# Kernel optimization log

Hardware: AMD Instinct MI355X
Metric: run time of the kernel (lower is better)

Reference implementation:

```python
import jax, jax.numpy as jnp
import numpy as np

# static config (mirrors init_kwargs)
FS = 512          # frame_seqlen
NFPB = 2          # num_frame_per_block
NIB = 3           # num image/action/state blocks
NAPB = 32         # num_action_per_block
NSPB = 1          # num_state_per_block
LOCAL = 4         # local_attn_size (frames)
FIRST = FS
IMGB = NIB * NFPB * FS
ALEN = NIB * NAPB
SLEN = NIB * NSPB
TOTAL = FIRST + IMGB + ALEN + SLEN   # 3683
DIM = 1536
NH = 12
HD = DIM // NH    # 128
EPS = 1e-6


def _build_mask():
    # faithful port of _visualize_attention_mask (the block-sparse pattern)
    m = np.zeros((TOTAL, TOTAL), dtype=bool)
    fi0, fi1 = 0, FIRST
    ib0, ib1 = fi1, fi1 + IMGB
    a0, a1 = ib1, ib1 + ALEN
    s0 = a1
    m[fi0:fi1, fi0:fi1] = True  # first image: self only (sink)
    for b in range(NIB):
        bs = ib0 + b * NFPB * FS
        be = ib0 + (b + 1) * NFPB * FS
        m[bs:be, fi0:fi1] = True                      # sink
        kv = max(ib0, be - LOCAL * FS)                # local window
        m[bs:be, kv:be] = True
        m[bs:be, a0 + b * NAPB:a0 + (b + 1) * NAPB] = True
        m[bs:be, s0 + b * NSPB:s0 + (b + 1) * NSPB] = True
    for b in range(NIB):
        ab0 = a0 + b * NAPB
        ab1 = a0 + (b + 1) * NAPB
        m[ab0:ab1, fi0:fi1] = True
        ibe = ib0 + (b + 1) * NFPB * FS
        kv = max(ib0, ibe - LOCAL * FS)
        m[ab0:ab1, kv:ibe] = True
        m[ab0:ab1, ab0:ab1] = True
        m[ab0:ab1, s0 + b * NSPB:s0 + (b + 1) * NSPB] = True
    for b in range(NIB):
        ss = s0 + b * NSPB
        se = s0 + (b + 1) * NSPB
        m[ss:se, ss:se] = True
    return m

_MASK = jnp.asarray(_build_mask())


def _rms_norm(x, g):
    # WanRMSNorm over full dim, fp32 accumulation
    v = jnp.mean(jnp.square(x.astype(jnp.float32)), axis=-1, keepdims=True)
    return (x.astype(jnp.float32) * jax.lax.rsqrt(v + EPS)).astype(x.dtype) * g


def _rope(x, cos, sin):
    # x: [B,L,n,hd]; pairs are consecutive (..., hd//2, 2)
    B, L, n, d = x.shape
    xp = x.reshape(B, L, n, d // 2, 2)
    xr, xi = xp[..., 0], xp[..., 1]
    c = cos[None, :, None, :]
    s = sin[None, :, None, :]
    yr = xr * c - xi * s
    yi = xr * s + xi * c
    return jnp.stack([yr, yi], axis=-1).reshape(B, L, n, d)


def setup_inputs() -> dict:
    key = jax.random.key(0)
    ks = jax.random.split(key, 16)
    x = jax.random.normal(ks[0], (1, TOTAL, DIM), jnp.float32)

    def mkfreq(k, L):
        ang = jax.random.uniform(k, (L, HD // 2), jnp.float32, 0.0, 2.0 * np.pi)
        return jnp.stack([jnp.cos(ang), jnp.sin(ang)], axis=-1).reshape(L, HD)

    freqs = mkfreq(ks[1], FIRST + IMGB)
    freqs_action = mkfreq(ks[2], ALEN)
    freqs_state = mkfreq(ks[3], SLEN)
    sc = 1.0 / np.sqrt(DIM)
    Wq = jax.random.normal(ks[4], (DIM, DIM), jnp.float32) * sc
    Wk = jax.random.normal(ks[5], (DIM, DIM), jnp.float32) * sc
    Wv = jax.random.normal(ks[6], (DIM, DIM), jnp.float32) * sc
    Wo = jax.random.normal(ks[7], (DIM, DIM), jnp.float32) * sc
    bq = jax.random.normal(ks[8], (DIM,), jnp.float32) * 0.01
    bk = jax.random.normal(ks[9], (DIM,), jnp.float32) * 0.01
    bv = jax.random.normal(ks[10], (DIM,), jnp.float32) * 0.01
    bo = jax.random.normal(ks[11], (DIM,), jnp.float32) * 0.01
    gq = jnp.ones((DIM,), jnp.float32)
    gk = jnp.ones((DIM,), jnp.float32)
    return {"x": x, "freqs": freqs, "freqs_action": freqs_action,
            "freqs_state": freqs_state, "Wq": Wq, "bq": bq, "Wk": Wk, "bk": bk,
            "Wv": Wv, "bv": bv, "Wo": Wo, "bo": bo, "gq": gq, "gk": gk}


def reference(x, freqs, freqs_action, freqs_state, Wq, bq, Wk, bk, Wv, bv, Wo, bo, gq, gk):
    B, L, _ = x.shape
    q = _rms_norm(x @ Wq + bq, gq).reshape(B, L, NH, HD)
    k = _rms_norm(x @ Wk + bk, gk).reshape(B, L, NH, HD)
    v = (x @ Wv + bv).reshape(B, L, NH, HD)
    # full-sequence rope: image freqs then action freqs then state freqs
    f = jnp.concatenate([freqs, freqs_action, freqs_state], axis=0).reshape(L, HD // 2, 2)
    cos, sin = f[..., 0], f[..., 1]
    q = _rope(q, cos, sin)
    k = _rope(k, cos, sin)
    scores = jnp.einsum('bqnd,bknd->bnqk', q, k) / np.sqrt(HD)
    scores = jnp.where(_MASK[None, None], scores, jnp.finfo(scores.dtype).min)
    p = jax.nn.softmax(scores, axis=-1)
    o = jnp.einsum('bnqk,bknd->bqnd', p, v).reshape(B, L, DIM)
    return o @ Wo + bo
```

## Files before the change

kernel.cpp:

```cpp
#include <hip/hip_runtime.h>

#define LSEQ 3683
#define LPAD 3840
#define DIMSZ 1536
#define NHEAD 12
#define HEADD 128
#define SM_SCALE 0.088388347648318447f

typedef unsigned short u16;
typedef unsigned int u32;
typedef __bf16 bf16x8 __attribute__((ext_vector_type(8)));
typedef float f32x4 __attribute__((ext_vector_type(4)));

__device__ __forceinline__ u16 f2b(float f) {
  u32 u = __float_as_uint(f);
  u += 0x7FFFu + ((u >> 16) & 1u);
  return (u16)(u >> 16);
}
__device__ __forceinline__ float b2f(u16 s) {
  return __uint_as_float(((u32)s) << 16);
}
__device__ __forceinline__ int imax(int a, int b) { return a > b ? a : b; }

__device__ __forceinline__ void gl_lds16(const u16* g, u16* l) {
  __builtin_amdgcn_global_load_lds((const __attribute__((address_space(1))) u32*)g,
                                   (__attribute__((address_space(3))) u32*)l,
                                   16, 0, 0);
}

__device__ __forceinline__ int xcd_swz(int orig, int nwg) {
  int q = nwg >> 3, r = nwg & 7;
  int x = orig & 7, l = orig >> 3;
  return (x < r ? x * (q + 1) : r * (q + 1) + (x - r) * q) + l;
}

#define CONV_BLOCKS 5760
__global__ void prep_kernel(const float* __restrict__ x, u16* __restrict__ xb,
                            const float* __restrict__ W0, const float* __restrict__ W1,
                            const float* __restrict__ W2, const float* __restrict__ W3,
                            u16* __restrict__ Wt) {
  __shared__ float tile[32][33];
  int bx = blockIdx.x;
  if (bx < CONV_BLOCKS) {
    long idx = (long)bx * blockDim.x + threadIdx.x;
    long base = idx * 4;
    if (base >= (long)LPAD * DIMSZ) return;
    float4 v;
    if (base < (long)LSEQ * DIMSZ) v = *(const float4*)(x + base);
    else v = make_float4(0.f, 0.f, 0.f, 0.f);
    ushort4 o;
    o.x = f2b(v.x); o.y = f2b(v.y); o.z = f2b(v.z); o.w = f2b(v.w);
    *(ushort4*)(xb + base) = o;
  } else {
    int i = bx - CONV_BLOCKS;
    int z = i / 2304;
    int r = i % 2304;
    int bxx = r % 48, byy = r / 48;
    const float* W = (z == 0) ? W0 : (z == 1) ? W1 : (z == 2) ? W2 : W3;
    u16* dst = Wt + (size_t)z * DIMSZ * DIMSZ;
    int k0 = bxx * 32, n0 = byy * 32;
    int tx = threadIdx.x & 31, ty = threadIdx.x >> 5;
    #pragma unroll
    for (int q = 0; q < 4; q++) {
      int k = k0 + ty + q * 8;
      tile[ty + q * 8][tx] = W[(size_t)k * DIMSZ + n0 + tx];
    }
    __syncthreads();
    #pragma unroll
    for (int q = 0; q < 4; q++) {
      int n = n0 + ty + q * 8;
      dst[(size_t)n * DIMSZ + k0 + tx] = f2b(tile[tx][ty + q * 8]);
    }
  }
}

#define BAR() __builtin_amdgcn_s_barrier()
#define LGK0() asm volatile("s_waitcnt lgkmcnt(0)" ::: "memory")
#define LGK8() asm volatile("s_waitcnt lgkmcnt(8)" ::: "memory")
#define VMC9() asm volatile("s_waitcnt vmcnt(9)" ::: "memory")
#define VMC6() asm volatile("s_waitcnt vmcnt(6)" ::: "memory")
#define VMC0() asm volatile("s_waitcnt vmcnt(0)" ::: "memory")
#define PRIO1() __builtin_amdgcn_s_setprio(1)
#define PRIO0() __builtin_amdgcn_s_setprio(0)

#define STG_A(buf, q, kt) \
  gl_lds16(gA + (size_t)((q) * 64) * DIMSZ + (kt), &Asg[buf][((q) * 64 + w * 8) * 64]);
#define STG_B(buf, q, kt) \
  gl_lds16(gB + (size_t)((q) * 64) * DIMSZ + (kt), &Bsg[buf][((q) * 64 + w * 8) * 64]);

#define LDA3(buf, mh) { \
  _Pragma("unroll") for (int mf = 0; mf < 3; mf++) { \
    int rb = (wm * 96 + (mh) * 48 + mf * 16) * 64; \
    Ar[mf * 2 + 0] = *(const bf16x8*)&Asg[buf][rb + off0]; \
    Ar[mf * 2 + 1] = *(const bf16x8*)&Asg[buf][rb + off1]; } }
#define LDB3(buf, nh) { \
  _Pragma("unroll") for (int nf = 0; nf < 3; nf++) { \
    int rb = (wn * 96 + (nh) * 48 + nf * 16) * 64; \
    Br[nh][nf * 2 + 0] = *(const bf16x8*)&Bsg[buf][rb + off0]; \
    Br[nh][nf * 2 + 1] = *(const bf16x8*)&Bsg[buf][rb + off1]; } }

#define MFMAQ3(mh, nh) { \
  _Pragma("unroll") for (int mf = 0; mf < 3; mf++) \
    _Pragma("unroll") for (int nf = 0; nf < 3; nf++) { \
      acc[(mh)*3+mf][(nh)*3+nf] = __builtin_amdgcn_mfma_f32_16x16x32_bf16(Ar[mf*2+0], Br[nh][nf*2+0], acc[(mh)*3+mf][(nh)*3+nf], 0, 0, 0); \
      acc[(mh)*3+mf][(nh)*3+nf] = __builtin_amdgcn_mfma_f32_16x16x32_bf16(Ar[mf*2+1], Br[nh][nf*2+1], acc[(mh)*3+mf][(nh)*3+nf], 0, 0, 0); } }

#define GEMM384_BODY() \
  STG_B(0, 0, 0) STG_B(0, 1, 0) STG_B(0, 2, 0) \
  STG_A(0, 0, 0) STG_A(0, 1, 0) STG_A(0, 2, 0) \
  STG_A(0, 3, 0) STG_A(0, 4, 0) STG_A(0, 5, 0) \
  STG_B(1, 0, 64) STG_B(1, 1, 64) STG_B(1, 2, 64) \
  STG_A(1, 0, 64) STG_A(1, 1, 64) STG_A(1, 2, 64) \
  STG_A(1, 3, 64) STG_A(1, 4, 64) STG_A(1, 5, 64) \
  VMC9(); \
  BAR(); \
  for (int i = 0; i < DIMSZ / 64 / 2 - 1; ++i) { \
    int kt2 = (2 * i + 2) * 64; \
    int kt3 = (2 * i + 3) * 64; \
    LDA3(0, 0) LDB3(0, 0) \
    LGK8(); BAR(); LGK0(); \
    PRIO1(); MFMAQ3(0, 0) PRIO0(); \
    BAR(); \
    LDB3(0, 1) \
    BAR(); LGK0(); \
    PRIO1(); MFMAQ3(0, 1) PRIO0(); \
    BAR(); \
    LDA3(0, 1) \
    STG_B(0, 0, kt2) STG_B(0, 1, kt2) STG_B(0, 2, kt2) \
    BAR(); LGK0(); \
    PRIO1(); MFMAQ3(1, 1) PRIO0(); \
    BAR(); \
    STG_A(0, 0, kt2) STG_A(0, 1, kt2) STG_A(0, 2, kt2) \
    VMC6(); BAR(); \
    PRIO1(); MFMAQ3(1, 0) PRIO0(); \
    BAR(); \
    LDA3(1, 0) LDB3(1, 0) \
    STG_A(0, 3, kt2) STG_A(0, 4, kt2) STG_A(0, 5, kt2) \
    LGK8(); BAR(); LGK0(); \
    PRIO1(); MFMAQ3(0, 0) PRIO0(); \
    BAR(); \
    LDB3(1, 1) \
    BAR(); LGK0(); \
    PRIO1(); MFMAQ3(0, 1) PRIO0(); \
    BAR(); \
    LDA3(1, 1) \
    STG_B(1, 0, kt3) STG_B(1, 1, kt3) STG_B(1, 2, kt3) \
    BAR(); LGK0(); \
    PRIO1(); MFMAQ3(1, 1) PRIO0(); \
    BAR(); \
    STG_A(1, 0, kt3) STG_A(1, 1, kt3) STG_A(1, 2, kt3) \
    STG_A(1, 3, kt3) STG_A(1, 4, kt3) STG_A(1, 5, kt3) \
    VMC9(); BAR(); \
    PRIO1(); MFMAQ3(1, 0) PRIO0(); \
    BAR(); \
  } \
  { \
    LDA3(0, 0) LDB3(0, 0) \
    LGK8(); BAR(); LGK0(); \
    PRIO1(); MFMAQ3(0, 0) PRIO0(); \
    BAR(); \
    LDB3(0, 1) \
    BAR(); LGK0(); \
    PRIO1(); MFMAQ3(0, 1) PRIO0(); \
    BAR(); \
    LDA3(0, 1) \
    BAR(); LGK0(); \
    PRIO1(); MFMAQ3(1, 1) PRIO0(); \
    BAR(); \
    VMC0(); BAR(); \
    PRIO1(); MFMAQ3(1, 0) PRIO0(); \
    BAR(); \
    LDA3(1, 0) LDB3(1, 0) \
    LGK8(); BAR(); LGK0(); \
    PRIO1(); MFMAQ3(0, 0) PRIO0(); \
    BAR(); \
    LDB3(1, 1) \
    BAR(); LGK0(); \
    PRIO1(); MFMAQ3(0, 1) PRIO0(); \
    BAR(); \
    LDA3(1, 1) \
    BAR(); LGK0(); \
    PRIO1(); MFMAQ3(1, 1) PRIO0(); \
    MFMAQ3(1, 0) \
  }

__launch_bounds__(512, 2)
__global__ void gemm_qkv384_kernel(const u16* __restrict__ A, const u16* __restrict__ Wt,
                                   const float* __restrict__ bq, const float* __restrict__ bk,
                                   const float* __restrict__ bv,
                                   u16* __restrict__ Qb, u16* __restrict__ Kb,
                                   u16* __restrict__ Vt) {
  __shared__ __align__(16) u16 Asg[2][384 * 64];
  __shared__ __align__(16) u16 Bsg[2][192 * 64];

  int wg = xcd_swz(blockIdx.x, 10 * 24);
  int nt = wg % 24;
  int m0 = (wg / 24) * 384;
  int which = nt >> 3;
  const float* bias = (which == 0) ? bq : (which == 1) ? bk : bv;

  int t = threadIdx.x;
  int lane = t & 63, w = t >> 6;
  int c = lane & 15, g = lane >> 4;
  int wm = w >> 1, wn = w & 1;

  int srow = t >> 3;
  int schunk = ((t & 7) ^ (srow & 7)) * 8;
  const u16* gA = A + (size_t)(m0 + srow) * DIMSZ + schunk;
  const u16* gB = Wt + (size_t)(nt * 192 + srow) * DIMSZ + schunk;

  int off0 = c * 64 + ((g) ^ (c & 7)) * 8;
  int off1 = c * 64 + ((g + 4) ^ (c & 7)) * 8;

  f32x4 acc[6][6];
  f32x4 zero = {0.f, 0.f, 0.f, 0.f};
  #pragma unroll
  for (int am = 0; am < 6; am++)
    #pragma unroll
    for (int an = 0; an < 6; an++) acc[am][an] = zero;
  bf16x8 Ar[6];
  bf16x8 Br[2][6];

  GEMM384_BODY()

  #pragma unroll
  for (int an = 0; an < 6; an++) {
    int ncol = (nt & 7) * 192 + wn * 96 + (an / 3) * 48 + (an % 3) * 16 + c;
    float bvv = bias[ncol];
    #pragma unroll
    for (int am = 0; am < 6; am++) {
      int rowb = m0 + wm * 96 + (am / 3) * 48 + (am % 3) * 16 + 4 * g;
      if (which == 2) {
        ushort4 pv;
        pv.x = f2b(acc[am][an][0] + bvv);
        pv.y = f2b(acc[am][an][1] + bvv);
        pv.z = f2b(acc[am][an][2] + bvv);
        pv.w = f2b(acc[am][an][3] + bvv);
        *(ushort4*)&Vt[(size_t)ncol * LPAD + rowb] = pv;
      } else {
        u16* P = (which == 1) ? Kb : Qb;
        #pragma unroll
        for (int r = 0; r < 4; r++)
          P[(size_t)(rowb + r) * DIMSZ + ncol] = f2b(acc[am][an][r] + bvv);
      }
    }
  }
}

__launch_bounds__(512, 2)
__global__ void gemm_out384_kernel(const u16* __restrict__ A, const u16* __restrict__ Bt,
                                   const float* __restrict__ bias, float* __restrict__ outF) {
  __shared__ __align__(16) u16 Asg[2][384 * 64];
  __shared__ __align__(16) u16 Bsg[2][192 * 64];

  int wg = xcd_swz(blockIdx.x, 10 * 8);
  int nt = wg % 8;
  int m0 = (wg / 8) * 384;

  int t = threadIdx.x;
  int lane = t & 63, w = t >> 6;
  int c = lane & 15, g = lane >> 4;
  int wm = w >> 1, wn = w & 1;

  int srow = t >> 3;
  int schunk = ((t & 7) ^ (srow & 7)) * 8;
  const u16* gA = A + (size_t)(m0 + srow) * DIMSZ + schunk;
  const u16* gB = Bt + (size_t)(nt * 192 + srow) * DIMSZ + schunk;

  int off0 = c * 64 + ((g) ^ (c & 7)) * 8;
  int off1 = c * 64 + ((g + 4) ^ (c & 7)) * 8;

  f32x4 acc[6][6];
  f32x4 zero = {0.f, 0.f, 0.f, 0.f};
  #pragma unroll
  for (int am = 0; am < 6; am++)
    #pragma unroll
    for (int an = 0; an < 6; an++) acc[am][an] = zero;
  bf16x8 Ar[6];
  bf16x8 Br[2][6];

  GEMM384_BODY()

  #pragma unroll
  for (int an = 0; an < 6; an++) {
    int ncol = nt * 192 + wn * 96 + (an / 3) * 48 + (an % 3) * 16 + c;
    float bvv = bias[ncol];
    #pragma unroll
    for (int am = 0; am < 6; am++) {
      int rowb = m0 + wm * 96 + (am / 3) * 48 + (am % 3) * 16 + 4 * g;
      #pragma unroll
      for (int r = 0; r < 4; r++) {
        int row = rowb + r;
        if (row < LSEQ) outF[(size_t)row * DIMSZ + ncol] = acc[am][an][r] + bvv;
      }
    }
  }
}

__launch_bounds__(256)
__global__ void normrope_kernel(u16* __restrict__ Qb, u16* __restrict__ Kb,
                                const float* __restrict__ gq, const float* __restrict__ gk,
                                const float* __restrict__ freqs, const float* __restrict__ freqs_a,
                                const float* __restrict__ freqs_s) {
  int l = blockIdx.x;
  int sel = blockIdx.y;
  u16* P = sel ? Kb : Qb;
  const float* gvec = sel ? gk : gq;
  int t = threadIdx.x;
  u16* row = P + (size_t)l * DIMSZ;
  float xv[6];
  #pragma unroll
  for (int i = 0; i < 3; i++) {
    int p = i * 256 + t;
    ushort2 u = *(const ushort2*)(row + 2 * p);
    xv[2 * i] = b2f(u.x);
    xv[2 * i + 1] = b2f(u.y);
  }
  float ss = 0.f;
  #pragma unroll
  for (int i = 0; i < 6; i++) ss += xv[i] * xv[i];
  #pragma unroll
  for (int d = 32; d; d >>= 1) ss += __shfl_down(ss, d);
  __shared__ float red[4];
  __shared__ float rshare;
  if ((t & 63) == 0) red[t >> 6] = ss;
  __syncthreads();
  if (t == 0) rshare = rsqrtf((red[0] + red[1] + red[2] + red[3]) * (1.0f / DIMSZ) + 1e-6f);
  __syncthreads();
  float rms = rshare;

  const float* f = (l < 3584) ? (freqs + (size_t)l * HEADD)
                : (l < 3680) ? (freqs_a + (size_t)(l - 3584) * HEADD)
                             : (freqs_s + (size_t)(l - 3680) * HEADD);
  #pragma unroll
  for (int i = 0; i < 3; i++) {
    int p = i * 256 + t;
    int j = p & 63;
    float2 csn = *(const float2*)(f + 2 * j);
    float2 gv = *(const float2*)(gvec + 2 * p);
    float xr = xv[2 * i] * rms * gv.x;
    float xi = xv[2 * i + 1] * rms * gv.y;
    ushort2 o;
    o.x = f2b(xr * csn.x - xi * csn.y);
    o.y = f2b(xr * csn.y + xi * csn.x);
    *(ushort2*)(row + 2 * p) = o;
  }
}

#define PSLOT_U16 16640
#define NTAIL 84
__launch_bounds__(256, 2)
__global__ void attn_fused_kernel(const u16* __restrict__ Q, const u16* __restrict__ K,
                                  const u16* __restrict__ Vt, u16* __restrict__ O,
                                  u16* __restrict__ DP, float* __restrict__ Part) {
  __shared__ __align__(16) u16 Ks[2][32 * 136];
  __shared__ __align__(16) u16 Vs[2][128 * 40];
  __shared__ __align__(16) u16 Pl[4][32 * 40];

  int t = threadIdx.x, lane = t & 63, w = t >> 6, g = lane >> 4, c = lane & 15;
  const float c1 = SM_SCALE * 1.44269504088896340f;
  const float c2 = 12.0f * 1.44269504088896340f;

  f32x4 zero = {0.f, 0.f, 0.f, 0.f};
  bf16x8 onesv;
  {
    u16 ob = 0x3F80;
    #pragma unroll
    for (int i = 0; i < 8; i++) onesv[i] = ((const __bf16*)&ob)[0];
  }

  if (blockIdx.x < NTAIL) {
    char* smem = (char*)&Ks[0][0];
    float* Lsum = (float*)(smem + 20608);

    int j = blockIdx.x;
    int bxx = j % 7;
    int h = j / 7;
    int qt, part;
    if (bxx < 3) { qt = 112 + bxx; part = 0; }
    else if (bxx < 6) { qt = 112 + (bxx - 3); part = 1; }
    else { qt = 115; part = 0; }
    int qbase = qt * 32;
    bool heavy = (qt <= 114);

    int S0, E0, S1, E1, S2, E2, S3, E3, niv;
    if (qbase < 3680) {
      int b = (qbase - 3584) >> 5;
      int ibe = 512 + (b + 1) * 1024;
      int kv = imax(512, ibe - 2048);
      S0 = 0; E0 = 512; S1 = kv; E1 = ibe;
      S2 = 3584 + 32 * b; E2 = S2 + 32; S3 = 3680 + b; E3 = S3 + 1; niv = 4;
    } else {
      S0 = 3680; E0 = 3683; S1 = S2 = S3 = 0; E1 = E2 = E3 = 0; niv = 1;
    }
    bool diag = (qbase >= 3680);

    int B0 = S0 & ~31, B1 = S1 & ~31, B2 = S2 & ~31, B3 = S3 & ~31;
    int T1 = (E0 - B0 + 31) >> 5;
    int T2 = T1 + ((niv > 1) ? ((E1 - B1 + 31) >> 5) : 0);
    int T3 = T2 + ((niv > 2) ? ((E2 - B2 + 31) >> 5) : 0);
    int T4 = T3 + ((niv > 3) ? ((E3 - B3 + 31) >> 5) : 0);
    int ntile = T4;

    int rlo = 0, rhi = ntile;
    if (heavy) { int half = (ntile + 1) >> 1; if (part == 0) rhi = half; else rlo = half; }

    auto tile_of = [&](int f, int& k0, int& lo, int& hi) {
      k0 = B0 + (f << 5); lo = S0; hi = E0;
      if (niv > 1 && f >= T1) { k0 = B1 + ((f - T1) << 5); lo = S1; hi = E1; }
      if (niv > 2 && f >= T2) { k0 = B2 + ((f - T2) << 5); lo = S2; hi = E2; }
      if (niv > 3 && f >= T3) { k0 = B3 + ((f - T3) << 5); lo = S3; hi = E3; }
    };

    bf16x8 qf[2][4];
    #pragma unroll
    for (int a = 0; a < 2; a++) {
      const u16* qp = Q + (size_t)(qbase + a * 16 + c) * DIMSZ + h * HEADD + 8 * g;
      #pragma unroll
      for (int s = 0; s < 4; s++) qf[a][s] = *(const bf16x8*)(qp + 32 * s);
    }

    f32x4 acc[2][8];
    f32x4 lacc[2];
    #pragma unroll
    for (int a = 0; a < 2; a++) {
      lacc[a] = zero;
      #pragma unroll
      for (int cc = 0; cc < 8; cc++) acc[a][cc] = zero;
    }

    u16* PwA = (u16*)smem + w * 2560;
    u16* PwB = PwA + 1280;

    bf16x8 kc[2][4], vbuf[8], pa0, pa1;

    auto loadK = [&](int k0) {
      #pragma unroll
      for (int k2 = 0; k2 < 2; k2++) {
        const u16* kp = K + (size_t)(k0 + 16 * k2 + c) * DIMSZ + h * HEADD + 8 * g;
        #pragma unroll
        for (int s = 0; s < 4; s++) kc[k2][s] = *(const bf16x8*)(kp + 32 * s);
      }
    };
    auto loadV = [&](int k0) {
      #pragma unroll
      for (int cc = 0; cc < 8; cc++)
        vbuf[cc] = *(const bf16x8*)(Vt + (size_t)(h * HEADD + cc * 16 + c) * LPAD + k0 + 8 * g);
    };
    auto QKf = [&](f32x4 (&sc)[2][2]) {
      sc[0][0] = zero; sc[0][1] = zero; sc[1][0] = zero; sc[1][1] = zero;
      #pragma unroll
      for (int k2 = 0; k2 < 2; k2++)
        #pragma unroll
        for (int s = 0; s < 4; s++) {
          sc[0][k2] = __builtin_amdgcn_mfma_f32_16x16x32_bf16(qf[0][s], kc[k2][s], sc[0][k2], 0, 0, 0);
          sc[1][k2] = __builtin_amdgcn_mfma_f32_16x16x32_bf16(qf[1][s], kc[k2][s], sc[1][k2], 0, 0, 0);
        }
    };
    auto smstore = [&](f32x4 (&sc)[2][2], int k0, int lo, int hi, u16* Pw) {
      #pragma unroll
      for (int a = 0; a < 2; a++)
        #pragma unroll
        for (int k2 = 0; k2 < 2; k2++) {
          int k = k0 + k2 * 16 + c;
          bool valid = (k >= lo) && (k < hi);
          #pragma unroll
          for (int r = 0; r < 4; r++) {
            float p = __builtin_amdgcn_exp2f(sc[a][k2][r] * c1 - c2);
            bool v = valid;
            if (diag) { int qr = qbase + a * 16 + 4 * g + r; v = v && (k == qr); }
            Pw[(a * 16 + 4 * g + r) * 40 + k2 * 16 + c] = v ? f2b(p) : (u16)0;
          }
        }
    };
    auto readP = [&](u16* Pw) {
      pa0 = *(const bf16x8*)&Pw[c * 40 + 8 * g];
      pa1 = *(const bf16x8*)&Pw[(16 + c) * 40 + 8 * g];
    };
    auto PV = [&]() {
      #pragma unroll
      for (int cc = 0; cc < 8; cc++) {
        acc[0][cc] = __builtin_amdgcn_mfma_f32_16x16x32_bf16(pa0, vbuf[cc], acc[0][cc], 0, 0, 0);
        acc[1][cc] = __builtin_amdgcn_mfma_f32_16x16x32_bf16(pa1, vbuf[cc], acc[1][cc], 0, 0, 0);
      }
      lacc[0] = __builtin_amdgcn_mfma_f32_16x16x32_bf16(pa0, onesv, lacc[0], 0, 0, 0);
      lacc[1] = __builtin_amdgcn_mfma_f32_16x16x32_bf16(pa1, onesv, lacc[1], 0, 0, 0);
    };

    int i = rlo + w;
    if (i < rhi) {
      int ik0, ilo, ihi; tile_of(i, ik0, ilo, ihi);
      loadK(ik0);
      loadV(ik0);
      {
        f32x4 sc[2][2]; QKf(sc);
        smstore(sc, ik0, ilo, ihi, PwA);
      }
      asm volatile("s_waitcnt lgkmcnt(0)" ::: "memory");
      __builtin_amdgcn_sched_barrier(0);
      readP(PwA);
      int nx = i + 4;
      int nk0 = 0, nlo = 0, nhi = 0;
      bool useB = true;
      if (nx < rhi) { tile_of(nx, nk0, nlo, nhi); loadK(nk0); }
      while (nx < rhi) {
        int ck0 = nk0, clo = nlo, chi = nhi;
        f32x4 sc[2][2]; QKf(sc);
        int nn = nx + 4;
        if (nn < rhi) { tile_of(nn, nk0, nlo, nhi); loadK(nk0); }
        u16* Pw = useB ? PwB : PwA;
        smstore(sc, ck0, clo, chi, Pw);
        PV();
        loadV(ck0);
        asm volatile("s_waitcnt lgkmcnt(0)" ::: "memory");
        __builtin_amdgcn_sched_barrier(0);
        readP(Pw);
        useB = !useB;
        i = nx; nx = nn;
      }
      PV();
    }

    __syncthreads();
    float* Oacc = (float*)smem;
    if (w == 0) {
      #pragma unroll
      for (int a = 0; a < 2; a++) {
        #pragma unroll
        for (int cc = 0; cc < 8; cc++)
          #pragma unroll
          for (int r = 0; r < 4; r++)
            Oacc[(a * 16 + 4 * g + r) * 132 + cc * 16 + c] = acc[a][cc][r];
        if (c == 0)
          #pragma unroll
          for (int r = 0; r < 4; r++) Lsum[a * 16 + 4 * g + r] = lacc[a][r];
      }
    }
    __syncthreads();
    #pragma unroll
    for (int ww = 1; ww < 4; ww++) {
      if (w == ww) {
        #pragma unroll
        for (int a = 0; a < 2; a++) {
          #pragma unroll
          for (int cc = 0; cc < 8; cc++)
            #pragma unroll
            for (int r = 0; r < 4; r++)
              Oacc[(a * 16 + 4 * g + r) * 132 + cc * 16 + c] += acc[a][cc][r];
          if (c == 0)
            #pragma unroll
            for (int r = 0; r < 4; r++) Lsum[a * 16 + 4 * g + r] += lacc[a][r];
        }
      }
      __syncthreads();
    }

    int row = t >> 3, c0 = (t & 7) * 16;
    if (heavy) {
      size_t slot = ((size_t)((qt - 112) * 12 + h)) * 2 + part;
      float* P = Part + slot * 4160;
      #pragma unroll
      for (int jj = 0; jj < 16; jj += 4)
        *(float4*)&P[row * 128 + c0 + jj] = *(float4*)&Oacc[row * 132 + c0 + jj];
      if ((t & 7) == 0) P[4096 + row] = Lsum[row];
    } else {
      int orow = qbase + row;
      if (orow < LSEQ) {
        float lsv = Lsum[row];
        float inv = (lsv > 0.f) ? 1.0f / lsv : 0.f;
        u16 tmp[16];
        #pragma unroll
        for (int jj = 0; jj < 16; jj++) tmp[jj] = f2b(Oacc[row * 132 + c0 + jj] * inv);
        u16* op = O + (size_t)orow * DIMSZ + h * HEADD + c0;
        *(uint4*)(op) = *(uint4*)&tmp[0];
        *(uint4*)(op + 8) = *(uint4*)&tmp[8];
      }
    }
    return;
  }

  int bx = blockIdx.x - NTAIL;
  int qbase, h, part, nparts, fb;
  if (bx < 48) { qbase = (bx / 12) * 128; h = bx % 12; part = 0; nparts = 1; fb = -1; }
  else if (bx < 336) { int i = bx - 48; int qb = i / 36; h = (i / 3) % 12; part = i % 3; nparts = 3; fb = 0; qbase = 512 + qb * 128; }
  else if (bx < 720) { int i = bx - 336; int qb = i / 48; h = (i / 4) % 12; part = i % 4; nparts = 4; fb = 1; qbase = 1536 + qb * 128; }
  else { int i = bx - 720; int qb = i / 48; h = (i / 4) % 12; part = i % 4; nparts = 4; fb = 2; qbase = 2560 + qb * 128; }

  int S0, E0, S1, E1, S2, E2, S3, E3, niv;
  if (fb < 0) { S0 = 0; E0 = 512; S1 = E1 = S2 = E2 = S3 = E3 = 0; niv = 1; }
  else {
    int be = 512 + (fb + 1) * 1024;
    int kv = imax(512, be - 2048);
    S0 = 0; E0 = 512; S1 = kv; E1 = be;
    S2 = 3584 + 32 * fb; E2 = S2 + 32; S3 = 3680 + fb; E3 = S3 + 1; niv = 4;
  }
  int B0 = S0 & ~31, B1 = S1 & ~31, B2 = S2 & ~31, B3 = S3 & ~31;
  int T1 = (E0 - B0 + 31) >> 5;
  int T2 = T1 + ((niv > 1) ? ((E1 - B1 + 31) >> 5) : 0);
  int T3 = T2 + ((niv > 2) ? ((E2 - B2 + 31) >> 5) : 0);
  int T4 = T3 + ((niv > 3) ? ((E3 - B3 + 31) >> 5) : 0);
  int ntile = T4;
  int rlo = (ntile * part) / nparts, rhi = (ntile * (part + 1)) / nparts;

  auto tile_of = [&](int f, int& k0, int& lo, int& hi) {
    k0 = B0 + (f << 5); lo = S0; hi = E0;
    if (niv > 1 && f >= T1) { k0 = B1 + ((f - T1) << 5); lo = S1; hi = E1; }
    if (niv > 2 && f >= T2) { k0 = B2 + ((f - T2) << 5); lo = S2; hi = E2; }
    if (niv > 3 && f >= T3) { k0 = B3 + ((f - T3) << 5); lo = S3; hi = E3; }
  };

  const u16* kgp = K + (size_t)(t >> 3) * DIMSZ + h * HEADD + 8 * (t & 7);
  int kds = (t >> 3) * 136 + 8 * (t & 7);
  const u16* vgp = Vt + ((size_t)h * HEADD + (t >> 1)) * LPAD + 16 * (t & 1);
  int vds = (t >> 1) * 40 + 16 * (t & 1);

  uint4 sk0, sk1, sv0, sv1;
  auto stage_load = [&](int k0) {
    const u16* kp = kgp + (size_t)k0 * DIMSZ;
    sk0 = *(const uint4*)(kp);
    sk1 = *(const uint4*)(kp + 64);
    sv0 = *(const uint4*)(vgp + k0);
    sv1 = *(const uint4*)(vgp + k0 + 8);
  };
  auto stage_write = [&](int buf) {
    *(uint4*)&Ks[buf][kds] = sk0;
    *(uint4*)&Ks[buf][kds + 64] = sk1;
    *(uint4*)&Vs[buf][vds] = sv0;
    *(uint4*)&Vs[buf][vds + 8] = sv1;
  };

  int qrow0 = qbase + 32 * w;
  bf16x8 qf[2][4];
  #pragma unroll
  for (int a = 0; a < 2; a++) {
    const u16* qp = Q + (size_t)(qrow0 + a * 16 + c) * DIMSZ + h * HEADD + 8 * g;
    #pragma unroll
    for (int s = 0; s < 4; s++) qf[a][s] = *(const bf16x8*)(qp + 32 * s);
  }

  f32x4 acc[2][8];
  f32x4 lacc[2];
  #pragma unroll
  for (int a = 0; a < 2; a++) {
    lacc[a] = zero;
    #pragma unroll
    for (int cc = 0; cc < 8; cc++) acc[a][cc] = zero;
  }

  u16* Pw = &Pl[w][0];
  __bf16* Pwh = (__bf16*)Pw;

  {
    int k0, lo, hi; tile_of(rlo, k0, lo, hi);
    stage_load(k0);
    stage_write(0);
  }
  __syncthreads();
  int cur = 0;

  for (int tt = rlo; tt < rhi; ++tt) {
    int ck0, clo, chi; tile_of(tt, ck0, clo, chi);
    bool pre = (tt + 1 < rhi);
    if (pre) { int nk0, nl, nh; tile_of(tt + 1, nk0, nl, nh); stage_load(nk0); }

    f32x4 sc[2][2];
    sc[0][0] = zero; sc[0][1] = zero; sc[1][0] = zero; sc[1][1] = zero;
    #pragma unroll
    for (int k2 = 0; k2 < 2; k2++)
      #pragma unroll
      for (int s = 0; s < 4; s++) {
        bf16x8 kf = *(const bf16x8*)&Ks[cur][(16 * k2 + c) * 136 + 32 * s + 8 * g];
        sc[0][k2] = __builtin_amdgcn_mfma_f32_16x16x32_bf16(qf[0][s], kf, sc[0][k2], 0, 0, 0);
        sc[1][k2] = __builtin_amdgcn_mfma_f32_16x16x32_bf16(qf[1][s], kf, sc[1][k2], 0, 0, 0);
      }

    if (ck0 >= clo && ck0 + 32 <= chi) {
      #pragma unroll
      for (int a = 0; a < 2; a++)
        #pragma unroll
        for (int k2 = 0; k2 < 2; k2++)
          #pragma unroll
          for (int r = 0; r < 4; r++) {
            float p = __builtin_amdgcn_exp2f(sc[a][k2][r] * c1 - c2);
            Pwh[(a * 16 + 4 * g + r) * 40 + k2 * 16 + c] = (__bf16)p;
          }
    } else {
      #pragma unroll
      for (int a = 0; a < 2; a++)
        #pragma unroll
        for (int k2 = 0; k2 < 2; k2++) {
          int k = ck0 + k2 * 16 + c;
          bool valid = (k >= clo) && (k < chi);
          #pragma unroll
          for (int r = 0; r < 4; r++) {
            float p = __builtin_amdgcn_exp2f(sc[a][k2][r] * c1 - c2);
            Pwh[(a * 16 + 4 * g + r) * 40 + k2 * 16 + c] = valid ? (__bf16)p : (__bf16)0.0f;
          }
        }
    }
    asm volatile("s_waitcnt lgkmcnt(0)" ::: "memory");
    __builtin_amdgcn_sched_barrier(0);

    bf16x8 pa0 = *(const bf16x8*)&Pw[c * 40 + 8 * g];
    bf16x8 pa1 = *(const bf16x8*)&Pw[(16 + c) * 40 + 8 * g];

    #pragma unroll
    for (int cc = 0; cc < 8; cc++) {
      bf16x8 vf = *(const bf16x8*)&Vs[cur][(cc * 16 + c) * 40 + 8 * g];
      acc[0][cc] = __builtin_amdgcn_mfma_f32_16x16x32_bf16(pa0, vf, acc[0][cc], 0, 0, 0);
      acc[1][cc] = __builtin_amdgcn_mfma_f32_16x16x32_bf16(pa1, vf, acc[1][cc], 0, 0, 0);
    }
    lacc[0] = __builtin_amdgcn_mfma_f32_16x16x32_bf16(pa0, onesv, lacc[0], 0, 0, 0);
    lacc[1] = __builtin_amdgcn_mfma_f32_16x16x32_bf16(pa1, onesv, lacc[1], 0, 0, 0);

    if (pre) stage_write(cur ^ 1);
    __syncthreads();
    cur ^= 1;
  }

  if (nparts == 1) {
    float inv[2][4];
    #pragma unroll
    for (int a = 0; a < 2; a++)
      #pragma unroll
      for (int r = 0; r < 4; r++) inv[a][r] = (lacc[a][r] > 0.f) ? 1.0f / lacc[a][r] : 0.f;
    #pragma unroll
    for (int a = 0; a < 2; a++)
      #pragma unroll
      for (int cc = 0; cc < 8; cc++)
        #pragma unroll
        for (int r = 0; r < 4; r++) {
          int row = qrow0 + a * 16 + 4 * g + r;
          O[(size_t)row * DIMSZ + h * HEADD + cc * 16 + c] = f2b(acc[a][cc][r] * inv[a][r]);
        }
  } else {
    int qb = (qbase - 512 - fb * 1024) >> 7;
    int sbase = (fb == 0) ? 0 : (fb == 1 ? 288 : 672);
    int slot = sbase + (qb * 12 + h) * nparts + part;
    u16* DPs = DP + (size_t)slot * PSLOT_U16;
    float* lout = (float*)(DPs + 16384);
    #pragma unroll
    for (int a = 0; a < 2; a++) {
      #pragma unroll
      for (int cc = 0; cc < 8; cc++)
        #pragma unroll
        for (int r = 0; r < 4; r++)
          DPs[(32 * w + a * 16 + 4 * g + r) * 128 + cc * 16 + c] = f2b(acc[a][cc][r]);
      if (c == 0)
        #pragma unroll
        for (int r = 0; r < 4; r++) lout[32 * w + a * 16 + 4 * g + r] = lacc[a][r];
    }
  }
}

__launch_bounds__(256)
__global__ void attn_merge_kernel(const u16* __restrict__ DP, const float* __restrict__ Part,
                                  u16* __restrict__ O) {
  int bx = blockIdx.x, h = blockIdx.y;
  int T = threadIdx.x;
  if (bx < 24) {
    int qi = bx;
    int fb = qi >> 3, qb = qi & 7;
    int nparts = (fb == 0) ? 3 : 4;
    int sbase = (fb == 0) ? 0 : (fb == 1 ? 288 : 672);
    int slot0 = sbase + (qb * 12 + h) * nparts;
    int qbase = 512 + fb * 1024 + qb * 128;
    int row = T >> 1, c0 = 64 * (T & 1);

    float sum[64];
    #pragma unroll
    for (int j = 0; j < 64; j++) sum[j] = 0.f;
    float l = 0.f;
    for (int p = 0; p < nparts; p++) {
      const u16* S = DP + (size_t)(slot0 + p) * PSLOT_U16;
      l += ((const float*)(S + 16384))[row];
      #pragma unroll
      for (int j = 0; j < 64; j += 8) {
        uint4 v = *(const uint4*)&S[row * 128 + c0 + j];
        const u16* pv = (const u16*)&v;
        #pragma unroll
        for (int q = 0; q < 8; q++) sum[j + q] += b2f(pv[q]);
      }
    }
    float inv = (l > 0.f) ? 1.0f / l : 0.f;
    u16 tmp[64];
    #pragma unroll
    for (int j = 0; j < 64; j++) tmp[j] = f2b(sum[j] * inv);
    u16* op = O + (size_t)(qbase + row) * DIMSZ + h * HEADD + c0;
    #pragma unroll
    for (int j = 0; j < 64; j += 8) *(uint4*)(op + j) = *(uint4*)&tmp[j];
  } else {
    int b = bx - 24;
    const float* A = Part + ((size_t)(b * 12 + h)) * 2 * 4160;
    const float* B = A + 4160;
    int row = T >> 3, c0 = (T & 7) * 16;
    float l = A[4096 + row] + B[4096 + row];
    float inv = (l > 0.f) ? 1.0f / l : 0.f;
    int orow = 3584 + b * 32 + row;
    u16 tmp[16];
    #pragma unroll
    for (int jj = 0; jj < 16; jj += 4) {
      float4 va = *(const float4*)&A[row * 128 + c0 + jj];
      float4 vb = *(const float4*)&B[row * 128 + c0 + jj];
      tmp[jj + 0] = f2b((va.x + vb.x) * inv);
      tmp[jj + 1] = f2b((va.y + vb.y) * inv);
      tmp[jj + 2] = f2b((va.z + vb.z) * inv);
      tmp[jj + 3] = f2b((va.w + vb.w) * inv);
    }
    u16* op = O + (size_t)orow * DIMSZ + h * HEADD + c0;
    *(uint4*)(op) = *(uint4*)&tmp[0];
    *(uint4*)(op + 8) = *(uint4*)&tmp[8];
  }
}

extern "C" void kernel_launch(void* const* d_in, const int* in_sizes, int n_in,
                              void* d_out, int out_size, void* d_ws, size_t ws_size,
                              hipStream_t stream) {
  (void)in_sizes; (void)n_in; (void)out_size; (void)ws_size;
  const float* x       = (const float*)d_in[0];
  const float* freqs   = (const float*)d_in[1];
  const float* freqs_a = (const float*)d_in[2];
  const float* freqs_s = (const float*)d_in[3];
  const float* Wq = (const float*)d_in[4];
  const float* bq = (const float*)d_in[5];
  const float* Wk = (const float*)d_in[6];
  const float* bk = (const float*)d_in[7];
  const float* Wv = (const float*)d_in[8];
  const float* bv = (const float*)d_in[9];
  const float* Wo = (const float*)d_in[10];
  const float* bo = (const float*)d_in[11];
  const float* gq = (const float*)d_in[12];
  const float* gk = (const float*)d_in[13];
  float* out = (float*)d_out;

  char* ws = (char*)d_ws;
  size_t off = 0;
  auto alloc = [&](size_t bytes) -> void* {
    void* p = ws + off;
    off += (bytes + 255) & ~(size_t)255;
    return p;
  };
  u16* xb   = (u16*)alloc((size_t)LPAD * DIMSZ * 2);
  u16* Wt   = (u16*)alloc((size_t)4 * DIMSZ * DIMSZ * 2);
  u16* Qb   = (u16*)alloc((size_t)LPAD * DIMSZ * 2);
  u16* Kb   = (u16*)alloc((size_t)LPAD * DIMSZ * 2);
  u16* Vt   = (u16*)alloc((size_t)DIMSZ * LPAD * 2);
  u16* Ob   = (u16*)alloc((size_t)LPAD * DIMSZ * 2);
  u16* DP   = (u16*)alloc((size_t)1056 * PSLOT_U16 * 2);
  float* PartT = (float*)alloc((size_t)3 * 12 * 2 * 4160 * 4);

  prep_kernel<<<dim3(CONV_BLOCKS + 9216), 256, 0, stream>>>(x, xb, Wq, Wk, Wv, Wo, Wt);

  gemm_qkv384_kernel<<<dim3(240), 512, 0, stream>>>(xb, Wt, bq, bk, bv, Qb, Kb, Vt);

  normrope_kernel<<<dim3(LSEQ, 2), 256, 0, stream>>>(Qb, Kb, gq, gk, freqs, freqs_a, freqs_s);

  attn_fused_kernel<<<dim3(NTAIL + 1104), 256, 0, stream>>>(Qb, Kb, Vt, Ob, DP, PartT);
  attn_merge_kernel<<<dim3(27, 12), 256, 0, stream>>>(DP, PartT, Ob);

  gemm_out384_kernel<<<dim3(80), 512, 0, stream>>>(Ob, Wt + 3 * (size_t)DIMSZ * DIMSZ, bo, out);
}
```

Baseline: 238.7 us.

## Drop software pipelining in attention loop to raise occupancy to three blocks

Replaces the software-pipelined K/V prefetch loop, which used double-buffered P tiles and a full 8-register V buffer, with a simple per-tile loop. V is loaded and consumed in two halves, and the launch bound is raised from 2 to 3 blocks per SM. The intent is to cut register pressure so more waves are resident and can hide memory latency. In exchange, the explicit overlap of the next tile's K load with current compute is lost, so global loads are now exposed inside each iteration.

```diff
diff --git a/kernel.cpp b/kernel.cpp
--- a/kernel.cpp
+++ b/kernel.cpp
@@ -349,7 +349,7 @@
 
 #define PSLOT_U16 16640
 #define NTAIL 84
-__launch_bounds__(256, 2)
+__launch_bounds__(256, 3)
 __global__ void attn_fused_kernel(const u16* __restrict__ Q, const u16* __restrict__ K,
                                   const u16* __restrict__ Vt, u16* __restrict__ O,
                                   u16* __restrict__ DP, float* __restrict__ Part) {
@@ -430,9 +430,8 @@
     }
 
     u16* PwA = (u16*)smem + w * 2560;
-    u16* PwB = PwA + 1280;
-
-    bf16x8 kc[2][4], vbuf[8], pa0, pa1;
+
+    bf16x8 kc[2][4], vbuf[4], pa0, pa1;
 
     auto loadK = [&](int k0) {
       #pragma unroll
@@ -442,10 +441,10 @@
         for (int s = 0; s < 4; s++) kc[k2][s] = *(const bf16x8*)(kp + 32 * s);
       }
     };
-    auto loadV = [&](int k0) {
-      #pragma unroll
-      for (int cc = 0; cc < 8; cc++)
-        vbuf[cc] = *(const bf16x8*)(Vt + (size_t)(h * HEADD + cc * 16 + c) * LPAD + k0 + 8 * g);
+    auto loadV4 = [&](int k0, int hh) {
+      #pragma unroll
+      for (int cc = 0; cc < 4; cc++)
+        vbuf[cc] = *(const bf16x8*)(Vt + (size_t)(h * HEADD + (hh * 4 + cc) * 16 + c) * LPAD + k0 + 8 * g);
     };
     auto QKf = [&](f32x4 (&sc)[2][2]) {
       sc[0][0] = zero; sc[0][1] = zero; sc[1][0] = zero; sc[1][1] = zero;
@@ -473,52 +472,27 @@
           }
         }
     };
-    auto readP = [&](u16* Pw) {
-      pa0 = *(const bf16x8*)&Pw[c * 40 + 8 * g];
-      pa1 = *(const bf16x8*)&Pw[(16 + c) * 40 + 8 * g];
+    auto PV4 = [&](int hh) {
+      #pragma unroll
+      for (int cc = 0; cc < 4; cc++) {
+        acc[0][hh * 4 + cc] = __builtin_amdgcn_mfma_f32_16x16x32_bf16(pa0, vbuf[cc], acc[0][hh * 4 + cc], 0, 0, 0);
+        acc[1][hh * 4 + cc] = __builtin_amdgcn_mfma_f32_16x16x32_bf16(pa1, vbuf[cc], acc[1][hh * 4 + cc], 0, 0, 0);
+      }
     };
-    auto PV = [&]() {
-      #pragma unroll
-      for (int cc = 0; cc < 8; cc++) {
-        acc[0][cc] = __builtin_amdgcn_mfma_f32_16x16x32_bf16(pa0, vbuf[cc], acc[0][cc], 0, 0, 0);
-        acc[1][cc] = __builtin_amdgcn_mfma_f32_16x16x32_bf16(pa1, vbuf[cc], acc[1][cc], 0, 0, 0);
-      }
+
+    for (int i = rlo + w; i < rhi; i += 4) {
+      int ik0, ilo, ihi; tile_of(i, ik0, ilo, ihi);
+      loadK(ik0);
+      f32x4 sc[2][2]; QKf(sc);
+      smstore(sc, ik0, ilo, ihi, PwA);
+      asm volatile("s_waitcnt lgkmcnt(0)" ::: "memory");
+      __builtin_amdgcn_sched_barrier(0);
+      pa0 = *(const bf16x8*)&PwA[c * 40 + 8 * g];
+      pa1 = *(const bf16x8*)&PwA[(16 + c) * 40 + 8 * g];
+      loadV4(ik0, 0); PV4(0);
+      loadV4(ik0, 1); PV4(1);
       lacc[0] = __builtin_amdgcn_mfma_f32_16x16x32_bf16(pa0, onesv, lacc[0], 0, 0, 0);
       lacc[1] = __builtin_amdgcn_mfma_f32_16x16x32_bf16(pa1, onesv, lacc[1], 0, 0, 0);
-    };
-
-    int i = rlo + w;
-    if (i < rhi) {
-      int ik0, ilo, ihi; tile_of(i, ik0, ilo, ihi);
-      loadK(ik0);
-      loadV(ik0);
-      {
-        f32x4 sc[2][2]; QKf(sc);
-        smstore(sc, ik0, ilo, ihi, PwA);
-      }
-      asm volatile("s_waitcnt lgkmcnt(0)" ::: "memory");
-      __builtin_amdgcn_sched_barrier(0);
-      readP(PwA);
-      int nx = i + 4;
-      int nk0 = 0, nlo = 0, nhi = 0;
-      bool useB = true;
-      if (nx < rhi) { tile_of(nx, nk0, nlo, nhi); loadK(nk0); }
-      while (nx < rhi) {
-        int ck0 = nk0, clo = nlo, chi = nhi;
-        f32x4 sc[2][2]; QKf(sc);
-        int nn = nx + 4;
-        if (nn < rhi) { tile_of(nn, nk0, nlo, nhi); loadK(nk0); }
-        u16* Pw = useB ? PwB : PwA;
-        smstore(sc, ck0, clo, chi, Pw);
-        PV();
-        loadV(ck0);
-        asm volatile("s_waitcnt lgkmcnt(0)" ::: "memory");
-        __builtin_amdgcn_sched_barrier(0);
-        readP(Pw);
-        useB = !useB;
-        i = nx; nx = nn;
-      }
-      PV();
     }
 
     __syncthreads();
```

After: 253.0 us. +6.0%, slower.

## Split-K the output projection GEMM across two workgroups with atomic accumulation

Applied to the files above, without the earlier changes.

The output projection GEMM now splits K=1536 into two halves, doubling the grid from 80 to 160 workgroups so more of the device's compute units are busy. Each half adds its partial tile into the fp32 output with atomicAdd, and only the first half adds the bias. A memset of the output is added at the start of the stream, so the result also depends on float atomic ordering and costs extra atomic traffic.

```diff
diff --git a/kernel.cpp b/kernel.cpp
--- a/kernel.cpp
+++ b/kernel.cpp
@@ -105,18 +105,18 @@
       acc[(mh)*3+mf][(nh)*3+nf] = __builtin_amdgcn_mfma_f32_16x16x32_bf16(Ar[mf*2+0], Br[nh][nf*2+0], acc[(mh)*3+mf][(nh)*3+nf], 0, 0, 0); \
       acc[(mh)*3+mf][(nh)*3+nf] = __builtin_amdgcn_mfma_f32_16x16x32_bf16(Ar[mf*2+1], Br[nh][nf*2+1], acc[(mh)*3+mf][(nh)*3+nf], 0, 0, 0); } }
 
-#define GEMM384_BODY() \
-  STG_B(0, 0, 0) STG_B(0, 1, 0) STG_B(0, 2, 0) \
-  STG_A(0, 0, 0) STG_A(0, 1, 0) STG_A(0, 2, 0) \
-  STG_A(0, 3, 0) STG_A(0, 4, 0) STG_A(0, 5, 0) \
-  STG_B(1, 0, 64) STG_B(1, 1, 64) STG_B(1, 2, 64) \
-  STG_A(1, 0, 64) STG_A(1, 1, 64) STG_A(1, 2, 64) \
-  STG_A(1, 3, 64) STG_A(1, 4, 64) STG_A(1, 5, 64) \
+#define GEMM384_BODY_K(kb, klen) \
+  STG_B(0, 0, (kb)) STG_B(0, 1, (kb)) STG_B(0, 2, (kb)) \
+  STG_A(0, 0, (kb)) STG_A(0, 1, (kb)) STG_A(0, 2, (kb)) \
+  STG_A(0, 3, (kb)) STG_A(0, 4, (kb)) STG_A(0, 5, (kb)) \
+  STG_B(1, 0, (kb) + 64) STG_B(1, 1, (kb) + 64) STG_B(1, 2, (kb) + 64) \
+  STG_A(1, 0, (kb) + 64) STG_A(1, 1, (kb) + 64) STG_A(1, 2, (kb) + 64) \
+  STG_A(1, 3, (kb) + 64) STG_A(1, 4, (kb) + 64) STG_A(1, 5, (kb) + 64) \
   VMC9(); \
   BAR(); \
-  for (int i = 0; i < DIMSZ / 64 / 2 - 1; ++i) { \
-    int kt2 = (2 * i + 2) * 64; \
-    int kt3 = (2 * i + 3) * 64; \
+  for (int i = 0; i < (klen) / 128 - 1; ++i) { \
+    int kt2 = (kb) + (2 * i + 2) * 64; \
+    int kt3 = (kb) + (2 * i + 3) * 64; \
     LDA3(0, 0) LDB3(0, 0) \
     LGK8(); BAR(); LGK0(); \
     PRIO1(); MFMAQ3(0, 0) PRIO0(); \
@@ -183,6 +183,8 @@
     PRIO1(); MFMAQ3(1, 1) PRIO0(); \
     MFMAQ3(1, 0) \
   }
+
+#define GEMM384_BODY() GEMM384_BODY_K(0, DIMSZ)
 
 __launch_bounds__(512, 2)
 __global__ void gemm_qkv384_kernel(const u16* __restrict__ A, const u16* __restrict__ Wt,
@@ -253,9 +255,11 @@
   __shared__ __align__(16) u16 Asg[2][384 * 64];
   __shared__ __align__(16) u16 Bsg[2][192 * 64];
 
-  int wg = xcd_swz(blockIdx.x, 10 * 8);
-  int nt = wg % 8;
-  int m0 = (wg / 8) * 384;
+  int wg = xcd_swz(blockIdx.x, 160);
+  int nt = (wg % 16) >> 1;
+  int ks = wg & 1;
+  int m0 = (wg / 16) * 384;
+  int kb = ks * 768;
 
   int t = threadIdx.x;
   int lane = t & 63, w = t >> 6;
@@ -279,19 +283,19 @@
   bf16x8 Ar[6];
   bf16x8 Br[2][6];
 
-  GEMM384_BODY()
+  GEMM384_BODY_K(kb, 768)
 
   #pragma unroll
   for (int an = 0; an < 6; an++) {
     int ncol = nt * 192 + wn * 96 + (an / 3) * 48 + (an % 3) * 16 + c;
-    float bvv = bias[ncol];
+    float bvv = (ks == 0) ? bias[ncol] : 0.f;
     #pragma unroll
     for (int am = 0; am < 6; am++) {
       int rowb = m0 + wm * 96 + (am / 3) * 48 + (am % 3) * 16 + 4 * g;
       #pragma unroll
       for (int r = 0; r < 4; r++) {
         int row = rowb + r;
-        if (row < LSEQ) outF[(size_t)row * DIMSZ + ncol] = acc[am][an][r] + bvv;
+        if (row < LSEQ) atomicAdd(&outF[(size_t)row * DIMSZ + ncol], acc[am][an][r] + bvv);
       }
     }
   }
@@ -849,6 +853,8 @@
   u16* DP   = (u16*)alloc((size_t)1056 * PSLOT_U16 * 2);
   float* PartT = (float*)alloc((size_t)3 * 12 * 2 * 4160 * 4);
 
+  hipMemsetAsync(out, 0, (size_t)LSEQ * DIMSZ * sizeof(float), stream);
+
   prep_kernel<<<dim3(CONV_BLOCKS + 9216), 256, 0, stream>>>(x, xb, Wq, Wk, Wv, Wo, Wt);
 
   gemm_qkv384_kernel<<<dim3(240), 512, 0, stream>>>(xb, Wt, bq, bk, bv, Qb, Kb, Vt);
@@ -858,5 +864,5 @@
   attn_fused_kernel<<<dim3(NTAIL + 1104), 256, 0, stream>>>(Qb, Kb, Vt, Ob, DP, PartT);
   attn_merge_kernel<<<dim3(27, 12), 256, 0, stream>>>(DP, PartT, Ob);
 
-  gemm_out384_kernel<<<dim3(80), 512, 0, stream>>>(Ob, Wt + 3 * (size_t)DIMSZ * DIMSZ, bo, out);
-}
+  gemm_out384_kernel<<<dim3(160), 512, 0, stream>>>(Ob, Wt + 3 * (size_t)DIMSZ * DIMSZ, bo, out);
+}
```

Result: slower. 256.7 us (+7.5%).
